# Kernel tuning notes

Hardware: AMD Instinct MI355X
Metric: run time of the kernel (lower is better)

The kernel has to match this reference:

```python
import jax, jax.numpy as jnp
import numpy as np

N = 500_000
B = 10_000
L = N // B  # 50 tokens per session
H = 128


def setup_inputs() -> dict:
    key = jax.random.key(0)
    ks = jax.random.split(key, 7)
    x = jax.random.normal(ks[0], (N, H), dtype=jnp.float32)
    # sorted segment ids: B sessions of length L (every segment non-empty)
    batch = jnp.repeat(jnp.arange(B, dtype=jnp.int32), L)
    # index of the last element of each session
    last_ixs = jnp.arange(B, dtype=jnp.int32) * L + (L - 1)
    s = 1.0 / np.sqrt(H)
    W1_w = jax.random.uniform(ks[1], (H, H), jnp.float32, -s, s)
    W1_b = jax.random.uniform(ks[2], (H,), jnp.float32, -s, s)
    W2_w = jax.random.uniform(ks[3], (H, H), jnp.float32, -s, s)
    W2_b = jax.random.uniform(ks[4], (H,), jnp.float32, -s, s)
    q_w = jax.random.uniform(ks[5], (1, H), jnp.float32, -s, s)
    q_b = jax.random.uniform(ks[6], (1,), jnp.float32, -s, s)
    return {"x": x, "W1_w": W1_w, "W1_b": W1_b, "W2_w": W2_w, "W2_b": W2_b,
            "q_w": q_w, "q_b": q_b, "batch": batch, "last_ixs": last_ixs,
            "num_segments": B}


def reference(x, W1_w, W1_b, W2_w, W2_b, q_w, q_b, batch, last_ixs, num_segments):
    # v_i = x[last_ixs]; repeat_interleave(v_i, bincount(batch)) == v_i[batch] (batch sorted)
    v_n_repeat = x[last_ixs][batch]                                   # [N, H]
    h = jax.nn.sigmoid(v_n_repeat @ W1_w.T + W1_b + x @ W2_w.T + W2_b)  # [N, H]
    e = (h @ q_w.T + q_b)[:, 0]                                       # [N]
    # segment-wise (per-session) numerically-stable softmax
    m = jax.ops.segment_max(e, batch, num_segments=num_segments)      # [B]
    z = jnp.exp(e - m[batch])                                         # [N]
    denom = jax.ops.segment_sum(z, batch, num_segments=num_segments)  # [B]
    alpha = (z / denom[batch])[:, None]                               # [N, 1]
    # scatter_add pooling of alpha * x over sessions
    s_g = jax.ops.segment_sum(alpha * x, batch, num_segments=num_segments)  # [B, H]
    return s_g
```

## Files before the change

### kernel.cpp

```cpp
#include <hip/hip_runtime.h>

#define H_DIM 128
#define L_SESS 50
#define B_SESS 10000
#define NBLK 1024
#define NITER 10
#define LDSTR 136
#define ESTR 5

typedef __bf16 bf16_t;
typedef __bf16 bf16x8 __attribute__((ext_vector_type(8)));
typedef float f32x4 __attribute__((ext_vector_type(4)));

__global__ __launch_bounds__(256) void cvt_kernel(
    const float* __restrict__ w2, const float* __restrict__ w1b,
    const float* __restrict__ w2bi, unsigned short* __restrict__ w2out,
    float* __restrict__ bias12) {
  int i = blockIdx.x * 256 + threadIdx.x;
  float4 v = ((const float4*)w2)[i];
  union { bf16_t h[4]; ushort4 u4; } tmp;
  tmp.h[0] = (bf16_t)v.x; tmp.h[1] = (bf16_t)v.y;
  tmp.h[2] = (bf16_t)v.z; tmp.h[3] = (bf16_t)v.w;
  *(ushort4*)(w2out + (size_t)4 * i) = tmp.u4;
  if (i < H_DIM) bias12[i] = w1b[i] + w2bi[i];
}

__global__ __launch_bounds__(256) void sess_u_kernel(
    const float* __restrict__ x, const float* __restrict__ w1,
    const float* __restrict__ bias12, float* __restrict__ U) {
  __shared__ __attribute__((aligned(16))) unsigned short W1s[H_DIM * LDSTR];
  __shared__ __attribute__((aligned(16))) unsigned short Vs[16 * LDSTR];
  const int t = threadIdx.x;
  const int s0 = blockIdx.x * 16;
  for (int i = t; i < 4096; i += 256) {
    float4 v = ((const float4*)w1)[i];
    int row = i >> 5, col = (i & 31) * 4;
    union { bf16_t h[4]; ushort4 u4; } tmp;
    tmp.h[0] = (bf16_t)v.x; tmp.h[1] = (bf16_t)v.y;
    tmp.h[2] = (bf16_t)v.z; tmp.h[3] = (bf16_t)v.w;
    *(ushort4*)&W1s[row * LDSTR + col] = tmp.u4;
  }
  for (int i = t; i < 512; i += 256) {
    int j = i >> 5, col = (i & 31) * 4;
    float4 v = ((const float4*)(x + ((size_t)(s0 + j) * L_SESS + (L_SESS - 1)) * H_DIM))[i & 31];
    union { bf16_t h[4]; ushort4 u4; } tmp;
    tmp.h[0] = (bf16_t)v.x; tmp.h[1] = (bf16_t)v.y;
    tmp.h[2] = (bf16_t)v.z; tmp.h[3] = (bf16_t)v.w;
    *(ushort4*)&Vs[j * LDSTR + col] = tmp.u4;
  }
  __syncthreads();
  const int lane = t & 63, w = t >> 6, q = lane >> 4, c = lane & 15;
  const int n0 = (w * 2) * 16 + c, n1 = (w * 2 + 1) * 16 + c;
  const f32x4 zero4 = {0.f, 0.f, 0.f, 0.f};
  f32x4 acc0 = zero4, acc1 = zero4;
#pragma unroll
  for (int kt = 0; kt < 4; ++kt) {
    bf16x8 a  = *(const bf16x8*)&Vs[c * LDSTR + kt * 32 + q * 8];
    bf16x8 b0 = *(const bf16x8*)&W1s[n0 * LDSTR + kt * 32 + q * 8];
    bf16x8 b1 = *(const bf16x8*)&W1s[n1 * LDSTR + kt * 32 + q * 8];
    acc0 = __builtin_amdgcn_mfma_f32_16x16x32_bf16(a, b0, acc0, 0, 0, 0);
    acc1 = __builtin_amdgcn_mfma_f32_16x16x32_bf16(a, b1, acc1, 0, 0, 0);
  }
  float bias0 = bias12[n0], bias1 = bias12[n1];
#pragma unroll
  for (int r = 0; r < 4; ++r) {
    int m = q * 4 + r;
    U[(size_t)(s0 + m) * H_DIM + n0] = acc0[r] + bias0;
    U[(size_t)(s0 + m) * H_DIM + n1] = acc1[r] + bias1;
  }
}

__global__ __launch_bounds__(256, 4) void sess_attn_kernel(
    const float* __restrict__ x, const unsigned short* __restrict__ W2b,
    const float* __restrict__ U, const float* __restrict__ qw,
    const float* __restrict__ qb, float* __restrict__ out) {
  __shared__ __attribute__((aligned(16))) unsigned short Xb[64 * LDSTR];
  __shared__ float epart[64 * ESTR];
  __shared__ float alpha_s[64];

  const int t = threadIdx.x;
  const int lane = t & 63, w = t >> 6, q = lane >> 4, c = lane & 15;
  const int n0 = w * 32 + c, n1 = n0 + 16;

  const bf16x8* W2v = (const bf16x8*)W2b;
  bf16x8 bw2[4][2];
#pragma unroll
  for (int kt = 0; kt < 4; ++kt) {
    bw2[kt][0] = W2v[(n0 * H_DIM + kt * 32 + q * 8) >> 3];
    bw2[kt][1] = W2v[(n1 * H_DIM + kt * 32 + q * 8) >> 3];
  }
  const float qn0 = qw[n0], qn1 = qw[n1], qbv = qb[0];

  int s = blockIdx.x;
  int sc = (s < B_SESS) ? s : (B_SESS - 1);
  const float4* xv = (const float4*)(x + (size_t)sc * (L_SESS * H_DIM));
  float4 v[6];
#pragma unroll
  for (int j = 0; j < 6; ++j) v[j] = xv[t + 256 * j];
  float4 v6;
  if (t < 64) v6 = xv[1536 + t];
  float unx0 = U[(size_t)sc * H_DIM + n0];
  float unx1 = U[(size_t)sc * H_DIM + n1];

  const f32x4 zero4 = {0.f, 0.f, 0.f, 0.f};

  for (int it = 0; it < NITER; ++it) {
    __syncthreads();
    const float u0 = unx0, u1 = unx1;

#pragma unroll
    for (int j = 0; j < 6; ++j) {
      int i = t + 256 * j;
      int row = i >> 5, col = (i & 31) * 4;
      union { bf16_t h[4]; ushort4 u4; } tmp;
      tmp.h[0] = (bf16_t)v[j].x; tmp.h[1] = (bf16_t)v[j].y;
      tmp.h[2] = (bf16_t)v[j].z; tmp.h[3] = (bf16_t)v[j].w;
      *(ushort4*)&Xb[row * LDSTR + col] = tmp.u4;
    }
    if (t < 64) {
      int i = 1536 + t;
      int row = i >> 5, col = (i & 31) * 4;
      union { bf16_t h[4]; ushort4 u4; } tmp;
      tmp.h[0] = (bf16_t)v6.x; tmp.h[1] = (bf16_t)v6.y;
      tmp.h[2] = (bf16_t)v6.z; tmp.h[3] = (bf16_t)v6.w;
      *(ushort4*)&Xb[row * LDSTR + col] = tmp.u4;
    }
    __syncthreads();

    if (it + 1 < NITER) {
      int sn = s + NBLK;
      int snc = (sn < B_SESS) ? sn : (B_SESS - 1);
      const float4* xn = (const float4*)(x + (size_t)snc * (L_SESS * H_DIM));
#pragma unroll
      for (int j = 0; j < 6; ++j) v[j] = xn[t + 256 * j];
      if (t < 64) v6 = xn[1536 + t];
      unx0 = U[(size_t)snc * H_DIM + n0];
      unx1 = U[(size_t)snc * H_DIM + n1];
    }

    f32x4 acc[4][2];
#pragma unroll
    for (int mt = 0; mt < 4; ++mt) { acc[mt][0] = zero4; acc[mt][1] = zero4; }
#pragma unroll
    for (int kt = 0; kt < 4; ++kt) {
      const int ko = kt * 32 + q * 8;
#pragma unroll
      for (int mt = 0; mt < 4; ++mt) {
        bf16x8 a = *(const bf16x8*)&Xb[(mt * 16 + c) * LDSTR + ko];
        acc[mt][0] = __builtin_amdgcn_mfma_f32_16x16x32_bf16(a, bw2[kt][0], acc[mt][0], 0, 0, 0);
        acc[mt][1] = __builtin_amdgcn_mfma_f32_16x16x32_bf16(a, bw2[kt][1], acc[mt][1], 0, 0, 0);
      }
    }

#pragma unroll
    for (int mt = 0; mt < 4; ++mt) {
#pragma unroll
      for (int r = 0; r < 4; ++r) {
        float t0 = acc[mt][0][r] + u0;
        float t1 = acc[mt][1][r] + u1;
        float h0 = 1.0f / (1.0f + __expf(-t0));
        float h1 = 1.0f / (1.0f + __expf(-t1));
        float p = h0 * qn0 + h1 * qn1;
#pragma unroll
        for (int off = 1; off <= 8; off <<= 1) p += __shfl_xor(p, off);
        if (c == 0) epart[(mt * 16 + q * 4 + r) * ESTR + w] = p;
      }
    }
    __syncthreads();

    if (t < 64) {
      float e = qbv;
#pragma unroll
      for (int j = 0; j < 4; ++j) e += epart[t * ESTR + j];
      float val = (t < L_SESS) ? e : -1.0e30f;
      float mx = val;
#pragma unroll
      for (int off = 32; off > 0; off >>= 1) mx = fmaxf(mx, __shfl_xor(mx, off));
      float z = (t < L_SESS) ? __expf(e - mx) : 0.f;
      float d = z;
#pragma unroll
      for (int off = 32; off > 0; off >>= 1) d += __shfl_xor(d, off);
      alpha_s[t] = z / d;
    }
    __syncthreads();

    if (t < H_DIM) {
      float acc_p = 0.f;
#pragma unroll
      for (int m = 0; m < L_SESS; ++m) {
        unsigned short pv = Xb[m * LDSTR + t];
        acc_p += alpha_s[m] * __uint_as_float(((unsigned int)pv) << 16);
      }
      if (s < B_SESS) out[(size_t)s * H_DIM + t] = acc_p;
    }
    s += NBLK;
  }
}

extern "C" void kernel_launch(void* const* d_in, const int* in_sizes, int n_in,
                              void* d_out, int out_size, void* d_ws, size_t ws_size,
                              hipStream_t stream) {
  const float* x    = (const float*)d_in[0];
  const float* w1   = (const float*)d_in[1];
  const float* w1b  = (const float*)d_in[2];
  const float* w2   = (const float*)d_in[3];
  const float* w2bi = (const float*)d_in[4];
  const float* qw   = (const float*)d_in[5];
  const float* qb   = (const float*)d_in[6];
  float* out = (float*)d_out;

  unsigned short* W2bf = (unsigned short*)d_ws;
  float* bias12 = (float*)((char*)d_ws + 32768);
  float* U = (float*)((char*)d_ws + 36864);

  cvt_kernel<<<16, 256, 0, stream>>>(w2, w1b, w2bi, W2bf, bias12);
  sess_u_kernel<<<B_SESS / 16, 256, 0, stream>>>(x, w1, bias12, U);
  sess_attn_kernel<<<NBLK, 256, 0, stream>>>(x, W2bf, U, qw, qb, out);
}
```

Baseline: 393.9 us.

## Fuse weight conversion and session-vector GEMM into single attention kernel

Removes the separate weight-conversion and per-session U-projection kernels, so each block converts W1/W2 to bf16 in registers and computes the last-token projection with extra MFMAs from the already-staged LDS tile. This drops two kernel launches and the global round trip for U. The cost is more register pressure (occupancy hint lowered to 3) and redundant per-block weight conversion. The grid also changes to 768 blocks × 14 iterations, which rebalances the persistent loop.

```diff
diff --git a/kernel.cpp b/kernel.cpp
--- a/kernel.cpp
+++ b/kernel.cpp
@@ -3,8 +3,8 @@
 #define H_DIM 128
 #define L_SESS 50
 #define B_SESS 10000
-#define NBLK 1024
-#define NITER 10
+#define NBLK 768
+#define NITER 14
 #define LDSTR 136
 #define ESTR 5
 
@@ -12,67 +12,17 @@
 typedef __bf16 bf16x8 __attribute__((ext_vector_type(8)));
 typedef float f32x4 __attribute__((ext_vector_type(4)));
 
-__global__ __launch_bounds__(256) void cvt_kernel(
-    const float* __restrict__ w2, const float* __restrict__ w1b,
-    const float* __restrict__ w2bi, unsigned short* __restrict__ w2out,
-    float* __restrict__ bias12) {
-  int i = blockIdx.x * 256 + threadIdx.x;
-  float4 v = ((const float4*)w2)[i];
-  union { bf16_t h[4]; ushort4 u4; } tmp;
-  tmp.h[0] = (bf16_t)v.x; tmp.h[1] = (bf16_t)v.y;
-  tmp.h[2] = (bf16_t)v.z; tmp.h[3] = (bf16_t)v.w;
-  *(ushort4*)(w2out + (size_t)4 * i) = tmp.u4;
-  if (i < H_DIM) bias12[i] = w1b[i] + w2bi[i];
+__device__ __forceinline__ bf16x8 cvt_bf8(float4 a, float4 b) {
+  bf16x8 r;
+  r[0] = (bf16_t)a.x; r[1] = (bf16_t)a.y; r[2] = (bf16_t)a.z; r[3] = (bf16_t)a.w;
+  r[4] = (bf16_t)b.x; r[5] = (bf16_t)b.y; r[6] = (bf16_t)b.z; r[7] = (bf16_t)b.w;
+  return r;
 }
 
-__global__ __launch_bounds__(256) void sess_u_kernel(
+__global__ __launch_bounds__(256, 3) void fused_attn_kernel(
     const float* __restrict__ x, const float* __restrict__ w1,
-    const float* __restrict__ bias12, float* __restrict__ U) {
-  __shared__ __attribute__((aligned(16))) unsigned short W1s[H_DIM * LDSTR];
-  __shared__ __attribute__((aligned(16))) unsigned short Vs[16 * LDSTR];
-  const int t = threadIdx.x;
-  const int s0 = blockIdx.x * 16;
-  for (int i = t; i < 4096; i += 256) {
-    float4 v = ((const float4*)w1)[i];
-    int row = i >> 5, col = (i & 31) * 4;
-    union { bf16_t h[4]; ushort4 u4; } tmp;
-    tmp.h[0] = (bf16_t)v.x; tmp.h[1] = (bf16_t)v.y;
-    tmp.h[2] = (bf16_t)v.z; tmp.h[3] = (bf16_t)v.w;
-    *(ushort4*)&W1s[row * LDSTR + col] = tmp.u4;
-  }
-  for (int i = t; i < 512; i += 256) {
-    int j = i >> 5, col = (i & 31) * 4;
-    float4 v = ((const float4*)(x + ((size_t)(s0 + j) * L_SESS + (L_SESS - 1)) * H_DIM))[i & 31];
-    union { bf16_t h[4]; ushort4 u4; } tmp;
-    tmp.h[0] = (bf16_t)v.x; tmp.h[1] = (bf16_t)v.y;
-    tmp.h[2] = (bf16_t)v.z; tmp.h[3] = (bf16_t)v.w;
-    *(ushort4*)&Vs[j * LDSTR + col] = tmp.u4;
-  }
-  __syncthreads();
-  const int lane = t & 63, w = t >> 6, q = lane >> 4, c = lane & 15;
-  const int n0 = (w * 2) * 16 + c, n1 = (w * 2 + 1) * 16 + c;
-  const f32x4 zero4 = {0.f, 0.f, 0.f, 0.f};
-  f32x4 acc0 = zero4, acc1 = zero4;
-#pragma unroll
-  for (int kt = 0; kt < 4; ++kt) {
-    bf16x8 a  = *(const bf16x8*)&Vs[c * LDSTR + kt * 32 + q * 8];
-    bf16x8 b0 = *(const bf16x8*)&W1s[n0 * LDSTR + kt * 32 + q * 8];
-    bf16x8 b1 = *(const bf16x8*)&W1s[n1 * LDSTR + kt * 32 + q * 8];
-    acc0 = __builtin_amdgcn_mfma_f32_16x16x32_bf16(a, b0, acc0, 0, 0, 0);
-    acc1 = __builtin_amdgcn_mfma_f32_16x16x32_bf16(a, b1, acc1, 0, 0, 0);
-  }
-  float bias0 = bias12[n0], bias1 = bias12[n1];
-#pragma unroll
-  for (int r = 0; r < 4; ++r) {
-    int m = q * 4 + r;
-    U[(size_t)(s0 + m) * H_DIM + n0] = acc0[r] + bias0;
-    U[(size_t)(s0 + m) * H_DIM + n1] = acc1[r] + bias1;
-  }
-}
-
-__global__ __launch_bounds__(256, 4) void sess_attn_kernel(
-    const float* __restrict__ x, const unsigned short* __restrict__ W2b,
-    const float* __restrict__ U, const float* __restrict__ qw,
+    const float* __restrict__ w1b, const float* __restrict__ w2,
+    const float* __restrict__ w2bi, const float* __restrict__ qw,
     const float* __restrict__ qb, float* __restrict__ out) {
   __shared__ __attribute__((aligned(16))) unsigned short Xb[64 * LDSTR];
   __shared__ float epart[64 * ESTR];
@@ -82,15 +32,6 @@
   const int lane = t & 63, w = t >> 6, q = lane >> 4, c = lane & 15;
   const int n0 = w * 32 + c, n1 = n0 + 16;
 
-  const bf16x8* W2v = (const bf16x8*)W2b;
-  bf16x8 bw2[4][2];
-#pragma unroll
-  for (int kt = 0; kt < 4; ++kt) {
-    bw2[kt][0] = W2v[(n0 * H_DIM + kt * 32 + q * 8) >> 3];
-    bw2[kt][1] = W2v[(n1 * H_DIM + kt * 32 + q * 8) >> 3];
-  }
-  const float qn0 = qw[n0], qn1 = qw[n1], qbv = qb[0];
-
   int s = blockIdx.x;
   int sc = (s < B_SESS) ? s : (B_SESS - 1);
   const float4* xv = (const float4*)(x + (size_t)sc * (L_SESS * H_DIM));
@@ -99,14 +40,26 @@
   for (int j = 0; j < 6; ++j) v[j] = xv[t + 256 * j];
   float4 v6;
   if (t < 64) v6 = xv[1536 + t];
-  float unx0 = U[(size_t)sc * H_DIM + n0];
-  float unx1 = U[(size_t)sc * H_DIM + n1];
+
+  bf16x8 bw2[4][2], bw1[4][2];
+  const float4* w2v = (const float4*)w2;
+  const float4* w1v = (const float4*)w1;
+#pragma unroll
+  for (int kt = 0; kt < 4; ++kt) {
+    const int ko4 = kt * 8 + q * 2;
+    bw2[kt][0] = cvt_bf8(w2v[n0 * 32 + ko4], w2v[n0 * 32 + ko4 + 1]);
+    bw2[kt][1] = cvt_bf8(w2v[n1 * 32 + ko4], w2v[n1 * 32 + ko4 + 1]);
+    bw1[kt][0] = cvt_bf8(w1v[n0 * 32 + ko4], w1v[n0 * 32 + ko4 + 1]);
+    bw1[kt][1] = cvt_bf8(w1v[n1 * 32 + ko4], w1v[n1 * 32 + ko4 + 1]);
+  }
+  const float qn0 = qw[n0], qn1 = qw[n1], qbv = qb[0];
+  const float b0 = w1b[n0] + w2bi[n0];
+  const float b1 = w1b[n1] + w2bi[n1];
 
   const f32x4 zero4 = {0.f, 0.f, 0.f, 0.f};
 
   for (int it = 0; it < NITER; ++it) {
     __syncthreads();
-    const float u0 = unx0, u1 = unx1;
 
 #pragma unroll
     for (int j = 0; j < 6; ++j) {
@@ -134,9 +87,17 @@
 #pragma unroll
       for (int j = 0; j < 6; ++j) v[j] = xn[t + 256 * j];
       if (t < 64) v6 = xn[1536 + t];
-      unx0 = U[(size_t)snc * H_DIM + n0];
-      unx1 = U[(size_t)snc * H_DIM + n1];
     }
+
+    f32x4 uacc0 = zero4, uacc1 = zero4;
+#pragma unroll
+    for (int kt = 0; kt < 4; ++kt) {
+      bf16x8 av = *(const bf16x8*)&Xb[49 * LDSTR + kt * 32 + q * 8];
+      uacc0 = __builtin_amdgcn_mfma_f32_16x16x32_bf16(av, bw1[kt][0], uacc0, 0, 0, 0);
+      uacc1 = __builtin_amdgcn_mfma_f32_16x16x32_bf16(av, bw1[kt][1], uacc1, 0, 0, 0);
+    }
+    const float u0 = uacc0[0] + b0;
+    const float u1 = uacc1[0] + b1;
 
     f32x4 acc[4][2];
 #pragma unroll
@@ -207,13 +168,6 @@
   const float* w2bi = (const float*)d_in[4];
   const float* qw   = (const float*)d_in[5];
   const float* qb   = (const float*)d_in[6];
-  float* out = (float*)d_out;
-
-  unsigned short* W2bf = (unsigned short*)d_ws;
-  float* bias12 = (float*)((char*)d_ws + 32768);
-  float* U = (float*)((char*)d_ws + 36864);
-
-  cvt_kernel<<<16, 256, 0, stream>>>(w2, w1b, w2bi, W2bf, bias12);
-  sess_u_kernel<<<B_SESS / 16, 256, 0, stream>>>(x, w1, bias12, U);
-  sess_attn_kernel<<<NBLK, 256, 0, stream>>>(x, W2bf, U, qw, qb, out);
+  fused_attn_kernel<<<NBLK, 256, 0, stream>>>(x, w1, w1b, w2, w2bi, qw, qb,
+                                              (float*)d_out);
 }
```

New measurement: 387.4 us. No clear change (-1.7%).
